# Kernel tuning notes

Measured on AMD Instinct MI355X. Metric: run time of the kernel, lower is better.

Reference implementation:

```python
import jax, jax.numpy as jnp
import numpy as np

N_NODES = 100000
N_EDGES = 1200000
IN_CH = 64
MID_CH = 256


def setup_inputs() -> dict:
    key = jax.random.key(0)
    ks = jax.random.split(key, 10)
    x = jax.random.normal(ks[0], (N_NODES, IN_CH), dtype=jnp.float32)
    edge_index = jax.random.randint(ks[1], (2, N_EDGES), 0, N_NODES, dtype=jnp.int64)
    conv_w = jax.random.normal(ks[2], (IN_CH, IN_CH), dtype=jnp.float32) * 0.1
    conv_b = jax.random.normal(ks[3], (IN_CH,), dtype=jnp.float32) * 0.1
    w1 = jax.random.normal(ks[4], (MID_CH, IN_CH), dtype=jnp.float32) * 0.1
    b1 = jax.random.normal(ks[5], (MID_CH,), dtype=jnp.float32) * 0.1
    w2 = jax.random.normal(ks[6], (MID_CH, MID_CH), dtype=jnp.float32) * 0.05
    b2 = jax.random.normal(ks[7], (MID_CH,), dtype=jnp.float32) * 0.05
    w3 = jax.random.normal(ks[8], (1, MID_CH), dtype=jnp.float32) * 0.05
    b3 = jax.random.normal(ks[9], (1,), dtype=jnp.float32) * 0.05
    return {"x": x, "edge_index": edge_index, "conv_w": conv_w, "conv_b": conv_b,
            "w1": w1, "b1": b1, "w2": w2, "b2": b2, "w3": w3, "b3": b3}


def gcn_conv(x, src, dst, n, conv_w, conv_b):
    # PyG GCNConv: linear transform, add self-loops, symmetric normalization,
    # scatter-sum aggregation at dst, then bias.
    loop = jnp.arange(n, dtype=src.dtype)
    s = jnp.concatenate([src, loop])
    d = jnp.concatenate([dst, loop])
    h = x @ conv_w.T  # [N, C]
    deg = jax.ops.segment_sum(jnp.ones_like(d, dtype=x.dtype), d, num_segments=n)
    dinv = jax.lax.rsqrt(deg)  # self-loops guarantee deg >= 1
    norm = dinv[s] * dinv[d]  # [E+N]
    msg = h[s] * norm[:, None]  # gather + scale
    agg = jax.ops.segment_sum(msg, d, num_segments=n)  # scatter-add
    return agg + conv_b


def reference(x, edge_index, conv_w, conv_b, w1, b1, w2, b2, w3, b3):
    n = x.shape[0]
    src, dst = edge_index[0], edge_index[1]
    out = jax.nn.relu(gcn_conv(x, src, dst, n, conv_w, conv_b))
    h = out + x  # residual
    h = jax.nn.relu(h @ w1.T + b1)
    h = jax.nn.relu(h @ w2.T + b2)
    return h @ w3.T + b3  # [N, 1]
```

## Files before the change

### kernel.cpp

```cpp
#include <hip/hip_runtime.h>


typedef __bf16 bf16x8 __attribute__((ext_vector_type(8)));
typedef float f32x4 __attribute__((ext_vector_type(4)));
typedef unsigned int u32x4 __attribute__((ext_vector_type(4)));
typedef unsigned short u16x4 __attribute__((ext_vector_type(4)));

#define NSLICE 8
#define EPB 2048
#define CAP 40

__device__ inline unsigned short f2b(float f) {
    unsigned int u = __builtin_bit_cast(unsigned int, f);
    u += 0x7fff + ((u >> 16) & 1);
    return (unsigned short)(u >> 16);
}

__device__ inline float blo(unsigned int v) {
    return __builtin_bit_cast(float, (v & 0xffffu) << 16);
}
__device__ inline float bhi(unsigned int v) {
    return __builtin_bit_cast(float, v & 0xffff0000u);
}

__device__ inline bf16x8 ld_frag16(const void* p) {
    u32x4 v = *(const u32x4*)p;
    return __builtin_bit_cast(bf16x8, v);
}

__global__ void k_fill(const int* __restrict__ src, const int* __restrict__ dst, int E,
                       int* __restrict__ cnt, int* __restrict__ csrf,
                       const float* __restrict__ w1, const float* __restrict__ w2,
                       unsigned short* __restrict__ w1b, unsigned short* __restrict__ w2b,
                       int sliceSz) {
    int bid = blockIdx.x;
    int t = threadIdx.x;
    if (bid < 256) {
        int i = bid * 256 + t;
        if (i < 16384) w1b[i] = f2b(w1[i]);
        w2b[i] = f2b(w2[i]);
    }
    int slice = bid & (NSLICE - 1);
    int chunk = bid >> 3;
    int lo = slice * sliceSz, hi = lo + sliceSz;
    int base = chunk * EPB;
    #pragma unroll
    for (int it = 0; it < EPB / 256; it++) {
        int i = base + it * 256 + t;
        if (i < E) {
            int d = dst[i];
            if (d >= lo && d < hi) {
                int pos = atomicAdd(&cnt[d], 1);
                if (pos < CAP) csrf[(size_t)d * CAP + pos] = src[i];
            }
        }
    }
}

__global__ __launch_bounds__(256) void k_gemm1(const float* __restrict__ x,
                                               const float* __restrict__ cw,
                                               const int* __restrict__ cnt,
                                               float* __restrict__ dinv,
                                               unsigned short* __restrict__ xb,
                                               unsigned short* __restrict__ h2, int N) {
    __shared__ float xt[64][64];
    int t = threadIdx.x;
    int lane = t & 63;
    int wv = t >> 6;
    int n0 = blockIdx.x * 64;

    float4 w[16];
    const float4* cw4 = (const float4*)(cw + lane * 64);
    #pragma unroll
    for (int i = 0; i < 16; i++) w[i] = cw4[i];

    const float4* x4 = (const float4*)x;
    float4* xt4 = (float4*)(&xt[0][0]);
    u16x4* xb4 = (u16x4*)xb;
    #pragma unroll
    for (int i = 0; i < 4; i++) {
        int idx = t + i * 256;
        int row = idx >> 4;
        int node = n0 + row;
        float4 v = make_float4(0.f, 0.f, 0.f, 0.f);
        if (node < N) {
            v = x4[(size_t)node * 16 + (idx & 15)];
            u16x4 vb;
            vb.x = f2b(v.x); vb.y = f2b(v.y); vb.z = f2b(v.z); vb.w = f2b(v.w);
            xb4[(size_t)node * 16 + (idx & 15)] = vb;
        }
        xt4[idx] = v;
    }
    __syncthreads();

    for (int nl = wv * 16; nl < wv * 16 + 16; ++nl) {
        int node = n0 + nl;
        if (node >= N) break;
        const float4* xr = (const float4*)(&xt[nl][0]);
        float a = 0.f;
        #pragma unroll
        for (int i = 0; i < 16; i++) {
            float4 xv = xr[i];
            a += w[i].x * xv.x; a += w[i].y * xv.y;
            a += w[i].z * xv.z; a += w[i].w * xv.w;
        }
        float dv = rsqrtf((float)(cnt[node] + 1));
        h2[(size_t)node * 64 + lane] = f2b(a * dv);
        if (lane == 0) dinv[node] = dv;
    }
}

__global__ __launch_bounds__(256) void k_agg(const unsigned short* __restrict__ h2,
                                             const int* __restrict__ csrf,
                                             const int* __restrict__ cnt,
                                             const float* __restrict__ dinv,
                                             const float* __restrict__ cb,
                                             const unsigned short* __restrict__ xb,
                                             unsigned short* __restrict__ hres, int N) {
    int t = threadIdx.x;
    int lane = t & 63;
    int wv = t >> 6;
    int d = blockIdx.x * 4 + wv;
    if (d >= N) return;
    int degTrue = cnt[d];
    int deg = degTrue > CAP ? CAP : degTrue;
    int half = lane >> 5;
    int ch = lane & 31;
    int cvec = d;
    if (lane < deg) cvec = csrf[(size_t)d * CAP + lane];

    const unsigned int* h2u = (const unsigned int*)h2;
    unsigned int sv = h2u[(size_t)d * 32 + ch];
    float a0 = 0.f, a1 = 0.f;
    if (half == 0) {
        a0 += blo(sv);
        a1 += bhi(sv);
    }
    for (int j = 0; j < deg; j += 16) {
        #pragma unroll
        for (int p = 0; p < 8; p++) {
            int e = j + 2 * p + half;
            int s = __shfl(cvec, e);
            unsigned int v = h2u[(size_t)s * 32 + ch];
            v = (e < deg) ? v : 0u;
            a0 += blo(v);
            a1 += bhi(v);
        }
    }
    a0 += __shfl_xor(a0, 32);
    a1 += __shfl_xor(a1, 32);
    float dv = dinv[d];
    float2 cbv = ((const float2*)cb)[ch];
    unsigned int xu = ((const unsigned int*)xb)[(size_t)d * 32 + ch];
    float o0 = fmaxf(a0 * dv + cbv.x, 0.f) + blo(xu);
    float o1 = fmaxf(a1 * dv + cbv.y, 0.f) + bhi(xu);
    if (half == 0) {
        unsigned int o = (unsigned int)f2b(o0) | ((unsigned int)f2b(o1) << 16);
        ((unsigned int*)hres)[(size_t)d * 32 + ch] = o;
    }
}

__global__ __launch_bounds__(512, 4) void k_mlp(const unsigned short* __restrict__ hres,
                                                const unsigned short* __restrict__ w1b,
                                                const float* __restrict__ b1,
                                                const unsigned short* __restrict__ w2b,
                                                const float* __restrict__ b2,
                                                const float* __restrict__ w3,
                                                const float* __restrict__ b3,
                                                float* __restrict__ out, int N) {
    __shared__ unsigned short h1t[32768];
    __shared__ unsigned short ht[8192];
    char* h1b = (char*)h1t;
    char* htb = (char*)ht;

    int t = threadIdx.x;
    int lane = t & 63;
    int wid = t >> 6;
    int wm = wid >> 2;
    int wn = wid & 3;
    int lr = lane & 15;
    int lk = (lane >> 4) * 8;
    int lg = lane >> 4;
    int n0 = blockIdx.x * 128;

    {
        const u16x4* hr4 = (const u16x4*)hres;
        #pragma unroll
        for (int i = 0; i < 4; i++) {
            int idx = t + i * 512;
            int row = idx >> 4;
            int c4 = idx & 15;
            int node = n0 + row;
            u16x4 v = {0, 0, 0, 0};
            if (node < N) v = hr4[(size_t)node * 16 + c4];
            int byte = (row << 7) + (c4 << 3);
            byte ^= (row & 7) << 4;
            *(u16x4*)(htb + byte) = v;
        }
    }
    __syncthreads();

    float bias1[4];
    #pragma unroll
    for (int nf = 0; nf < 4; nf++) bias1[nf] = b1[wn * 64 + nf * 16 + lr];

    f32x4 acc[4][4];
    #pragma unroll
    for (int mf = 0; mf < 4; mf++)
        #pragma unroll
        for (int nf = 0; nf < 4; nf++) {
            acc[mf][nf][0] = bias1[nf]; acc[mf][nf][1] = bias1[nf];
            acc[mf][nf][2] = bias1[nf]; acc[mf][nf][3] = bias1[nf];
        }

    #pragma unroll
    for (int kk = 0; kk < 2; kk++) {
        bf16x8 af[4], bfg[4];
        #pragma unroll
        for (int mf = 0; mf < 4; mf++) {
            int row = wm * 64 + mf * 16 + lr;
            int byte = (row << 7) + ((kk * 32 + lk) << 1);
            byte ^= (row & 7) << 4;
            af[mf] = ld_frag16(htb + byte);
        }
        #pragma unroll
        for (int nf = 0; nf < 4; nf++) {
            int c = wn * 64 + nf * 16 + lr;
            bfg[nf] = ld_frag16(w1b + c * 64 + kk * 32 + lk);
        }
        #pragma unroll
        for (int mf = 0; mf < 4; mf++)
            #pragma unroll
            for (int nf = 0; nf < 4; nf++)
                acc[mf][nf] = __builtin_amdgcn_mfma_f32_16x16x32_bf16(af[mf], bfg[nf], acc[mf][nf], 0, 0, 0);
    }

    #pragma unroll
    for (int mf = 0; mf < 4; mf++)
        #pragma unroll
        for (int nf = 0; nf < 4; nf++)
            #pragma unroll
            for (int r = 0; r < 4; r++) {
                int row = wm * 64 + mf * 16 + lg * 4 + r;
                int col = wn * 64 + nf * 16 + lr;
                float v = fmaxf(acc[mf][nf][r], 0.f);
                int byte = (row << 9) + (col << 1);
                byte ^= (row & 7) << 4;
                *(unsigned short*)(h1b + byte) = f2b(v);
            }
    __syncthreads();

    float bias2[4];
    #pragma unroll
    for (int nf = 0; nf < 4; nf++) bias2[nf] = b2[wn * 64 + nf * 16 + lr];
    #pragma unroll
    for (int mf = 0; mf < 4; mf++)
        #pragma unroll
        for (int nf = 0; nf < 4; nf++) {
            acc[mf][nf][0] = bias2[nf]; acc[mf][nf][1] = bias2[nf];
            acc[mf][nf][2] = bias2[nf]; acc[mf][nf][3] = bias2[nf];
        }

    #pragma unroll
    for (int kk = 0; kk < 8; kk++) {
        bf16x8 af[4], bfg[4];
        #pragma unroll
        for (int nf = 0; nf < 4; nf++) {
            int j = wn * 64 + nf * 16 + lr;
            bfg[nf] = ld_frag16(w2b + j * 256 + kk * 32 + lk);
        }
        #pragma unroll
        for (int mf = 0; mf < 4; mf++) {
            int row = wm * 64 + mf * 16 + lr;
            int byte = (row << 9) + ((kk * 32 + lk) << 1);
            byte ^= (row & 7) << 4;
            af[mf] = ld_frag16(h1b + byte);
        }
        #pragma unroll
        for (int mf = 0; mf < 4; mf++)
            #pragma unroll
            for (int nf = 0; nf < 4; nf++)
                acc[mf][nf] = __builtin_amdgcn_mfma_f32_16x16x32_bf16(af[mf], bfg[nf], acc[mf][nf], 0, 0, 0);
    }

    float w3v[4];
    #pragma unroll
    for (int nf = 0; nf < 4; nf++) w3v[nf] = w3[wn * 64 + nf * 16 + lr];

    float* red = (float*)htb;
    __syncthreads();

    #pragma unroll
    for (int mf = 0; mf < 4; mf++)
        #pragma unroll
        for (int r = 0; r < 4; r++) {
            float p = 0.f;
            #pragma unroll
            for (int nf = 0; nf < 4; nf++)
                p += fmaxf(acc[mf][nf][r], 0.f) * w3v[nf];
            p += __shfl_xor(p, 1);
            p += __shfl_xor(p, 2);
            p += __shfl_xor(p, 4);
            p += __shfl_xor(p, 8);
            if (lr == 0) {
                int row = wm * 64 + mf * 16 + lg * 4 + r;
                red[wn * 128 + row] = p;
            }
        }
    __syncthreads();

    if (t < 128) {
        int node = n0 + t;
        if (node < N) {
            float s = b3[0] + red[t] + red[128 + t] + red[256 + t] + red[384 + t];
            out[node] = s;
        }
    }
}

extern "C" void kernel_launch(void* const* d_in, const int* in_sizes, int n_in,
                              void* d_out, int out_size, void* d_ws, size_t ws_size,
                              hipStream_t stream) {
    const float* x  = (const float*)d_in[0];
    const int*   ei = (const int*)d_in[1];
    const float* cw = (const float*)d_in[2];
    const float* cb = (const float*)d_in[3];
    const float* w1 = (const float*)d_in[4];
    const float* b1 = (const float*)d_in[5];
    const float* w2 = (const float*)d_in[6];
    const float* b2 = (const float*)d_in[7];
    const float* w3 = (const float*)d_in[8];
    const float* b3 = (const float*)d_in[9];
    float* out = (float*)d_out;

    int N = in_sizes[0] / 64;
    int E = in_sizes[1] / 2;
    const int* src = ei;
    const int* dst = ei + E;

    char* ws = (char*)d_ws;
    size_t off = 0;
    auto alloc = [&](size_t bytes) {
        off = (off + 255) & ~(size_t)255;
        char* p = ws + off;
        off += bytes;
        return p;
    };
    int*            cnt   = (int*)alloc((size_t)N * 4);
    int*            csrf  = (int*)alloc((size_t)N * CAP * 4);
    float*          dinv  = (float*)alloc((size_t)N * 4);
    unsigned short* xb    = (unsigned short*)alloc((size_t)N * 64 * 2);
    unsigned short* h2    = (unsigned short*)alloc((size_t)N * 64 * 2);
    unsigned short* hresb = (unsigned short*)alloc((size_t)N * 64 * 2);
    unsigned short* w1b   = (unsigned short*)alloc((size_t)16384 * 2);
    unsigned short* w2b   = (unsigned short*)alloc((size_t)65536 * 2);
    (void)ws_size; (void)n_in; (void)out_size;

    hipMemsetAsync(cnt, 0, (size_t)N * 4, stream);

    int sliceSz = (N + NSLICE - 1) / NSLICE;
    int chunks = (E + EPB - 1) / EPB;
    k_fill<<<chunks * NSLICE, 256, 0, stream>>>(src, dst, E, cnt, csrf,
                                                w1, w2, w1b, w2b, sliceSz);

    k_gemm1<<<(N + 63) / 64, 256, 0, stream>>>(x, cw, cnt, dinv, xb, h2, N);

    k_agg<<<(N + 3) / 4, 256, 0, stream>>>(h2, csrf, cnt, dinv, cb, xb, hresb, N);

    k_mlp<<<(N + 127) / 128, 512, 0, stream>>>(hresb, w1b, b1, w2b, b2, w3, b3, out, N);
}
```

Measured before the change: 261.6 us.

## Vectorize edge fill reads, move weight conversion, prefetch MLP weight fragments

The edge-bucketing kernel now loads destination indices as int4 and processes four edges per thread, which cuts the number of load instructions. The bf16 conversion of w1/w2 moves from the fill kernel into the first GEMM kernel. The MLP kernel hoists its bias and w3 loads and preloads the first w1 fragments before the shared-memory staging. It also double-buffers the w2 fragments so the next k-step's loads overlap the current MFMAs. The vector load assumes E is a multiple of 4 (the tail is dropped otherwise), and holding the extra fragments raises register pressure.

```diff
diff --git a/kernel.cpp b/kernel.cpp
--- a/kernel.cpp
+++ b/kernel.cpp
@@ -29,29 +29,28 @@
 }
 
 __global__ void k_fill(const int* __restrict__ src, const int* __restrict__ dst, int E,
-                       int* __restrict__ cnt, int* __restrict__ csrf,
-                       const float* __restrict__ w1, const float* __restrict__ w2,
-                       unsigned short* __restrict__ w1b, unsigned short* __restrict__ w2b,
-                       int sliceSz) {
+                       int* __restrict__ cnt, int* __restrict__ csrf, int sliceSz) {
     int bid = blockIdx.x;
     int t = threadIdx.x;
-    if (bid < 256) {
-        int i = bid * 256 + t;
-        if (i < 16384) w1b[i] = f2b(w1[i]);
-        w2b[i] = f2b(w2[i]);
-    }
     int slice = bid & (NSLICE - 1);
     int chunk = bid >> 3;
     int lo = slice * sliceSz, hi = lo + sliceSz;
-    int base = chunk * EPB;
-    #pragma unroll
-    for (int it = 0; it < EPB / 256; it++) {
-        int i = base + it * 256 + t;
-        if (i < E) {
-            int d = dst[i];
-            if (d >= lo && d < hi) {
-                int pos = atomicAdd(&cnt[d], 1);
-                if (pos < CAP) csrf[(size_t)d * CAP + pos] = src[i];
+    int base4 = (chunk * EPB) >> 2;
+    const int4* dst4 = (const int4*)dst;
+    int E4 = E >> 2;
+    #pragma unroll
+    for (int it = 0; it < EPB / 1024; it++) {
+        int i4 = base4 + it * 256 + t;
+        if (i4 < E4) {
+            int4 d4 = dst4[i4];
+            int i0 = i4 << 2;
+            #pragma unroll
+            for (int q = 0; q < 4; q++) {
+                int d = (q == 0) ? d4.x : (q == 1) ? d4.y : (q == 2) ? d4.z : d4.w;
+                if (d >= lo && d < hi) {
+                    int pos = atomicAdd(&cnt[d], 1);
+                    if (pos < CAP) csrf[(size_t)d * CAP + pos] = src[i0 + q];
+                }
             }
         }
     }
@@ -60,11 +59,20 @@
 __global__ __launch_bounds__(256) void k_gemm1(const float* __restrict__ x,
                                                const float* __restrict__ cw,
                                                const int* __restrict__ cnt,
+                                               const float* __restrict__ w1,
+                                               const float* __restrict__ w2,
+                                               unsigned short* __restrict__ w1b,
+                                               unsigned short* __restrict__ w2b,
                                                float* __restrict__ dinv,
                                                unsigned short* __restrict__ xb,
                                                unsigned short* __restrict__ h2, int N) {
     __shared__ float xt[64][64];
     int t = threadIdx.x;
+    int gi = blockIdx.x * 256 + t;
+    if (gi < 65536) {
+        if (gi < 16384) w1b[gi] = f2b(w1[gi]);
+        w2b[gi] = f2b(w2[gi]);
+    }
     int lane = t & 63;
     int wv = t >> 6;
     int n0 = blockIdx.x * 64;
@@ -183,6 +191,18 @@
     int lg = lane >> 4;
     int n0 = blockIdx.x * 128;
 
+    float bias1[4], bias2[4], w3v[4];
+    #pragma unroll
+    for (int nf = 0; nf < 4; nf++) {
+        bias1[nf] = b1[wn * 64 + nf * 16 + lr];
+        bias2[nf] = b2[wn * 64 + nf * 16 + lr];
+        w3v[nf]  = w3[wn * 64 + nf * 16 + lr];
+    }
+    bf16x8 w1f0[4];
+    #pragma unroll
+    for (int nf = 0; nf < 4; nf++)
+        w1f0[nf] = ld_frag16(w1b + (wn * 64 + nf * 16 + lr) * 64 + lk);
+
     {
         const u16x4* hr4 = (const u16x4*)hres;
         #pragma unroll
@@ -200,10 +220,6 @@
     }
     __syncthreads();
 
-    float bias1[4];
-    #pragma unroll
-    for (int nf = 0; nf < 4; nf++) bias1[nf] = b1[wn * 64 + nf * 16 + lr];
-
     f32x4 acc[4][4];
     #pragma unroll
     for (int mf = 0; mf < 4; mf++)
@@ -216,17 +232,16 @@
     #pragma unroll
     for (int kk = 0; kk < 2; kk++) {
         bf16x8 af[4], bfg[4];
+        #pragma unroll
+        for (int nf = 0; nf < 4; nf++)
+            bfg[nf] = (kk == 0) ? w1f0[nf]
+                    : ld_frag16(w1b + (wn * 64 + nf * 16 + lr) * 64 + kk * 32 + lk);
         #pragma unroll
         for (int mf = 0; mf < 4; mf++) {
             int row = wm * 64 + mf * 16 + lr;
             int byte = (row << 7) + ((kk * 32 + lk) << 1);
             byte ^= (row & 7) << 4;
             af[mf] = ld_frag16(htb + byte);
-        }
-        #pragma unroll
-        for (int nf = 0; nf < 4; nf++) {
-            int c = wn * 64 + nf * 16 + lr;
-            bfg[nf] = ld_frag16(w1b + c * 64 + kk * 32 + lk);
         }
         #pragma unroll
         for (int mf = 0; mf < 4; mf++)
@@ -248,11 +263,13 @@
                 byte ^= (row & 7) << 4;
                 *(unsigned short*)(h1b + byte) = f2b(v);
             }
-    __syncthreads();
-
-    float bias2[4];
-    #pragma unroll
-    for (int nf = 0; nf < 4; nf++) bias2[nf] = b2[wn * 64 + nf * 16 + lr];
+
+    bf16x8 bcur[4];
+    #pragma unroll
+    for (int nf = 0; nf < 4; nf++)
+        bcur[nf] = ld_frag16(w2b + (wn * 64 + nf * 16 + lr) * 256 + lk);
+    __syncthreads();
+
     #pragma unroll
     for (int mf = 0; mf < 4; mf++)
         #pragma unroll
@@ -263,12 +280,13 @@
 
     #pragma unroll
     for (int kk = 0; kk < 8; kk++) {
-        bf16x8 af[4], bfg[4];
-        #pragma unroll
-        for (int nf = 0; nf < 4; nf++) {
-            int j = wn * 64 + nf * 16 + lr;
-            bfg[nf] = ld_frag16(w2b + j * 256 + kk * 32 + lk);
-        }
+        bf16x8 bnxt[4];
+        if (kk < 7) {
+            #pragma unroll
+            for (int nf = 0; nf < 4; nf++)
+                bnxt[nf] = ld_frag16(w2b + (wn * 64 + nf * 16 + lr) * 256 + (kk + 1) * 32 + lk);
+        }
+        bf16x8 af[4];
         #pragma unroll
         for (int mf = 0; mf < 4; mf++) {
             int row = wm * 64 + mf * 16 + lr;
@@ -280,12 +298,10 @@
         for (int mf = 0; mf < 4; mf++)
             #pragma unroll
             for (int nf = 0; nf < 4; nf++)
-                acc[mf][nf] = __builtin_amdgcn_mfma_f32_16x16x32_bf16(af[mf], bfg[nf], acc[mf][nf], 0, 0, 0);
-    }
-
-    float w3v[4];
-    #pragma unroll
-    for (int nf = 0; nf < 4; nf++) w3v[nf] = w3[wn * 64 + nf * 16 + lr];
+                acc[mf][nf] = __builtin_amdgcn_mfma_f32_16x16x32_bf16(af[mf], bcur[nf], acc[mf][nf], 0, 0, 0);
+        #pragma unroll
+        for (int nf = 0; nf < 4; nf++) bcur[nf] = bnxt[nf];
+    }
 
     float* red = (float*)htb;
     __syncthreads();
@@ -360,10 +376,10 @@
 
     int sliceSz = (N + NSLICE - 1) / NSLICE;
     int chunks = (E + EPB - 1) / EPB;
-    k_fill<<<chunks * NSLICE, 256, 0, stream>>>(src, dst, E, cnt, csrf,
-                                                w1, w2, w1b, w2b, sliceSz);
-
-    k_gemm1<<<(N + 63) / 64, 256, 0, stream>>>(x, cw, cnt, dinv, xb, h2, N);
+    k_fill<<<chunks * NSLICE, 256, 0, stream>>>(src, dst, E, cnt, csrf, sliceSz);
+
+    k_gemm1<<<(N + 63) / 64, 256, 0, stream>>>(x, cw, cnt, w1, w2, w1b, w2b,
+                                               dinv, xb, h2, N);
 
     k_agg<<<(N + 3) / 4, 256, 0, stream>>>(h2, csrf, cnt, dinv, cb, xb, hresb, N);
 
```

After: 265.9 us. No clear change (+1.6%).
